# Performance work log

Measured on AMD Instinct MI355X. Metric: run time of the kernel, lower is better.

Reference implementation:

```python
import jax, jax.numpy as jnp
import numpy as np

EMBED_DIM = 1024
NUM_HEADS = 16
N = 32768


def setup_inputs() -> dict:
    key = jax.random.key(0)
    k1, k2, k3 = jax.random.split(key, 3)
    h = jax.random.normal(k1, (N, EMBED_DIM), dtype=jnp.float32)
    # torch nn.Linear(E, 3E): weight [3E, E], bias [3E] (bias=True by default)
    W_qkv = jax.random.normal(k2, (3 * EMBED_DIM, EMBED_DIM), dtype=jnp.float32) * 0.02
    b_qkv = jax.random.normal(k3, (3 * EMBED_DIM,), dtype=jnp.float32) * 0.02
    return {"h": h, "W_qkv": W_qkv, "b_qkv": b_qkv}


def reference(h, W_qkv, b_qkv):
    n, e = h.shape
    head_dim = e // NUM_HEADS
    # fused QKV projection: [N, 3E]
    qkv = h @ W_qkv.T + b_qkv
    # reshape [N, 3, H, D] -> split
    qkv = qkv.reshape(n, 3, NUM_HEADS, head_dim)
    q, k, v = qkv[:, 0], qkv[:, 1], qkv[:, 2]  # each [N, H, D]
    # NOTE: attention over the HEAD axis per token, scaled by sqrt(embed_dim)
    scores = jnp.einsum("nid,njd->nij", q, k) / (e ** 0.5)  # [N, H, H]
    attn = jax.nn.softmax(scores, axis=-1)
    out = jnp.einsum("nij,njd->nid", attn, v)  # [N, H, D]
    # faithful to torch: permute(1,0,2) then reshape(N, E) (mixes node order)
    out = jnp.transpose(out, (1, 0, 2)).reshape(n, e)
    return out
```

## Files before the change

kernel.cpp:

```cpp
#include <hip/hip_runtime.h>
#include <stdint.h>

#define NTOK 32768
#define EMB  1024
#define QKVN 3072
#define NH   16
#define HD   64

typedef __bf16 bf16x8 __attribute__((ext_vector_type(8)));
typedef float  floatx4 __attribute__((ext_vector_type(4)));
typedef unsigned int   uintx4   __attribute__((ext_vector_type(4)));
typedef unsigned short ushortx4 __attribute__((ext_vector_type(4)));
typedef unsigned short ushortx8 __attribute__((ext_vector_type(8)));

__device__ __forceinline__ unsigned short f2bf_rne(float f){
    unsigned int x; __builtin_memcpy(&x, &f, 4);
    x += 0x7fffu + ((x >> 16) & 1u);
    return (unsigned short)(x >> 16);
}

__device__ __forceinline__ void async_copy16(void* lds, const void* gsrc){
    __builtin_amdgcn_global_load_lds(
        (const __attribute__((address_space(1))) unsigned int*)gsrc,
        (__attribute__((address_space(3))) unsigned int*)lds,
        16, 0, 0);
}

__global__ __launch_bounds__(256) void cast_f32_bf16(const float* __restrict__ in,
                                                     unsigned short* __restrict__ out,
                                                     int n4){
    int idx = blockIdx.x * 256 + threadIdx.x;
    if (idx < n4){
        floatx4 v = ((const floatx4*)in)[idx];
        ushortx4 o;
        o[0] = f2bf_rne(v[0]); o[1] = f2bf_rne(v[1]);
        o[2] = f2bf_rne(v[2]); o[3] = f2bf_rne(v[3]);
        ((ushortx4*)out)[idx] = o;
    }
}

__global__ __launch_bounds__(256) void qkv_gemm(const unsigned short* __restrict__ A,
                                                const unsigned short* __restrict__ B,
                                                const float* __restrict__ bias,
                                                unsigned short* __restrict__ C){
    __shared__ unsigned short As[128 * 32];
    __shared__ unsigned short Bs[128 * 32];

    const int tid  = threadIdx.x;
    const int m0   = blockIdx.y * 128;
    const int n0   = blockIdx.x * 128;
    const int lane = tid & 63;
    const int wave = tid >> 6;
    const int wm   = (wave >> 1) * 64;
    const int wn   = (wave & 1) * 64;
    const int r16  = lane & 15;
    const int quad = lane >> 4;

    floatx4 acc[4][4];
    #pragma unroll
    for (int mi = 0; mi < 4; mi++)
        #pragma unroll
        for (int ni = 0; ni < 4; ni++)
            acc[mi][ni] = floatx4{0.f, 0.f, 0.f, 0.f};

    for (int kt = 0; kt < EMB; kt += 32){
        #pragma unroll
        for (int s = 0; s < 2; s++){
            int c   = tid + s * 256;
            int row = c >> 2;
            int k8  = (c & 3) * 8;
            async_copy16(&As[c * 8], &A[(size_t)(m0 + row) * EMB + kt + k8]);
            async_copy16(&Bs[c * 8], &B[(size_t)(n0 + row) * EMB + kt + k8]);
        }
        __syncthreads();

        bf16x8 af[4], bb[4];
        #pragma unroll
        for (int mi = 0; mi < 4; mi++)
            af[mi] = *(const bf16x8*)&As[(wm + mi * 16 + r16) * 32 + quad * 8];
        #pragma unroll
        for (int ni = 0; ni < 4; ni++)
            bb[ni] = *(const bf16x8*)&Bs[(wn + ni * 16 + r16) * 32 + quad * 8];
        #pragma unroll
        for (int mi = 0; mi < 4; mi++)
            #pragma unroll
            for (int ni = 0; ni < 4; ni++)
                acc[mi][ni] = __builtin_amdgcn_mfma_f32_16x16x32_bf16(
                                  af[mi], bb[ni], acc[mi][ni], 0, 0, 0);
        __syncthreads();
    }

    #pragma unroll
    for (int ni = 0; ni < 4; ni++){
        int gcol = n0 + wn + ni * 16 + r16;
        float bv = bias[gcol];
        #pragma unroll
        for (int mi = 0; mi < 4; mi++){
            #pragma unroll
            for (int r = 0; r < 4; r++){
                int grow = m0 + wm + mi * 16 + quad * 4 + r;
                C[(size_t)grow * QKVN + gcol] = f2bf_rne(acc[mi][ni][r] + bv);
            }
        }
    }
}

#define TOKL 3072
#define KOFF 0
#define VOFF 1152
#define POFF 2688

__global__ __launch_bounds__(256) void attn_mfma(const unsigned short* __restrict__ qkv,
                                                 float* __restrict__ out){
    __shared__ unsigned short sm[4 * TOKL];

    const int tid = threadIdx.x;
    const int n0  = blockIdx.x * 4;

    #pragma unroll
    for (int s = 0; s < 2; s++){
        int c   = tid + s * 256;
        int t   = c >> 7;
        int rem = c & 127;
        int j   = rem >> 3;
        int d8  = (rem & 7) * 8;
        ushortx8 kk = *(const ushortx8*)&qkv[(size_t)(n0 + t) * QKVN + EMB + j * HD + d8];
        *(ushortx8*)&sm[t * TOKL + KOFF + j * 72 + d8] = kk;
        ushortx8 vv = *(const ushortx8*)&qkv[(size_t)(n0 + t) * QKVN + 2 * EMB + j * HD + d8];
        #pragma unroll
        for (int e = 0; e < 8; e++)
            sm[t * TOKL + VOFF + (d8 + e) * 24 + j] = vv[e];
    }
    __syncthreads();

    const int wave = tid >> 6;
    const int lane = tid & 63;
    const int col  = lane & 15;
    const int quad = lane >> 4;
    const int n    = n0 + wave;
    unsigned short* tb = &sm[wave * TOKL];

    const unsigned short* qrow = qkv + (size_t)n * QKVN + col * HD;
    bf16x8 qf0 = *(const bf16x8*)(qrow + quad * 8);
    bf16x8 qf1 = *(const bf16x8*)(qrow + 32 + quad * 8);
    bf16x8 kf0 = *(const bf16x8*)&tb[KOFF + col * 72 + quad * 8];
    bf16x8 kf1 = *(const bf16x8*)&tb[KOFF + col * 72 + 32 + quad * 8];

    floatx4 sAcc = floatx4{0.f, 0.f, 0.f, 0.f};
    sAcc = __builtin_amdgcn_mfma_f32_16x16x32_bf16(qf0, kf0, sAcc, 0, 0, 0);
    sAcc = __builtin_amdgcn_mfma_f32_16x16x32_bf16(qf1, kf1, sAcc, 0, 0, 0);

    #pragma unroll
    for (int r = 0; r < 4; r++){
        float sv = sAcc[r] * 0.03125f;
        float m = sv;
        m = fmaxf(m, __shfl_xor(m, 1));
        m = fmaxf(m, __shfl_xor(m, 2));
        m = fmaxf(m, __shfl_xor(m, 4));
        m = fmaxf(m, __shfl_xor(m, 8));
        float p = __expf(sv - m);
        float l = p;
        l += __shfl_xor(l, 1);
        l += __shfl_xor(l, 2);
        l += __shfl_xor(l, 4);
        l += __shfl_xor(l, 8);
        p *= 1.f / l;
        tb[POFF + (quad * 4 + r) * 24 + col] = f2bf_rne(p);
    }

    bf16x8 pf;
    #pragma unroll
    for (int z = 0; z < 8; z++) pf[z] = (__bf16)0.0f;
    if (quad < 2) pf = *(const bf16x8*)&tb[POFF + col * 24 + quad * 8];

    #pragma unroll
    for (int dblk = 0; dblk < 4; dblk++){
        bf16x8 vf;
        #pragma unroll
        for (int z = 0; z < 8; z++) vf[z] = (__bf16)0.0f;
        if (quad < 2) vf = *(const bf16x8*)&tb[VOFF + (dblk * 16 + col) * 24 + quad * 8];
        floatx4 o = __builtin_amdgcn_mfma_f32_16x16x32_bf16(
                        pf, vf, floatx4{0.f, 0.f, 0.f, 0.f}, 0, 0, 0);
        #pragma unroll
        for (int r = 0; r < 4; r++){
            int i = quad * 4 + r;
            out[(size_t)i * (NTOK * HD) + (size_t)n * HD + dblk * 16 + col] = o[r];
        }
    }
}

extern "C" void kernel_launch(void* const* d_in, const int* in_sizes, int n_in,
                              void* d_out, int out_size, void* d_ws, size_t ws_size,
                              hipStream_t stream){
    const float* h = (const float*)d_in[0];
    const float* W = (const float*)d_in[1];
    const float* b = (const float*)d_in[2];
    float* out = (float*)d_out;

    char* ws = (char*)d_ws;
    unsigned short* h_bf = (unsigned short*)ws;
    unsigned short* w_bf = (unsigned short*)(ws + (size_t)64 * 1024 * 1024);
    unsigned short* qkv  = (unsigned short*)(ws + (size_t)72 * 1024 * 1024);

    cast_f32_bf16<<<(NTOK * EMB / 4 + 255) / 256, 256, 0, stream>>>(h, h_bf, NTOK * EMB / 4);
    cast_f32_bf16<<<(QKVN * EMB / 4 + 255) / 256, 256, 0, stream>>>(W, w_bf, QKVN * EMB / 4);

    dim3 ggrid(QKVN / 128, NTOK / 128);
    qkv_gemm<<<ggrid, 256, 0, stream>>>(h_bf, w_bf, b, qkv);

    attn_mfma<<<NTOK / 4, 256, 0, stream>>>(qkv, out);
}
```

Before: 524.3 us.

## Replace QKV GEMM with 256x256 double-buffered pipelined MFMA kernel

Swaps the 128x128 single-buffered GEMM for a 256x256-tile kernel with 512 threads, BK=64, XOR-swizzled LDS, and double-buffered async global-to-LDS loads. Loads are interleaved with MFMA phases under s_setprio, and the block order is swizzled for L2 locality. The aim is to hide global memory latency and cut LDS bank conflicts in the main GEMM. In exchange it uses 128KB of dynamic LDS and hand-written waitcnt and barrier scheduling that is fragile to get right.

```diff
diff --git a/kernel.cpp b/kernel.cpp
--- a/kernel.cpp
+++ b/kernel.cpp
@@ -39,66 +39,167 @@
     }
 }
 
-__global__ __launch_bounds__(256) void qkv_gemm(const unsigned short* __restrict__ A,
-                                                const unsigned short* __restrict__ B,
-                                                const float* __restrict__ bias,
-                                                unsigned short* __restrict__ C){
-    __shared__ unsigned short As[128 * 32];
-    __shared__ unsigned short Bs[128 * 32];
-
-    const int tid  = threadIdx.x;
-    const int m0   = blockIdx.y * 128;
-    const int n0   = blockIdx.x * 128;
+
+__device__ __forceinline__ void stage_a_half(unsigned short* At, const unsigned short* A,
+                                             int m0, int h, int kt, int tid){
+    #pragma unroll
+    for (int g = 0; g < 2; g++){
+        int row0  = g * 128 + h * 64;
+        int rl    = tid >> 3;
+        int chunk = tid & 7;
+        int row   = row0 + rl;
+        int k8    = chunk ^ (row & 7);
+        async_copy16((char*)At + row0 * 128 + tid * 16,
+                     &A[(size_t)(m0 + row) * EMB + kt + k8 * 8]);
+    }
+}
+
+__device__ __forceinline__ void stage_b_half(unsigned short* Bt, const unsigned short* B,
+                                             int n0, int h, int kt, int tid){
+    #pragma unroll
+    for (int j = 0; j < 2; j++){
+        int qg    = j * 2 + (tid >> 8);
+        int row0  = qg * 64 + h * 32;
+        int t2    = tid & 255;
+        int rl    = t2 >> 3;
+        int chunk = tid & 7;
+        int row   = row0 + rl;
+        int k8    = chunk ^ (row & 7);
+        async_copy16((char*)Bt + row0 * 128 + t2 * 16,
+                     &B[(size_t)(n0 + row) * EMB + kt + k8 * 8]);
+    }
+}
+
+#define LDA_HALF(H)                                                                 \
+    _Pragma("unroll")                                                               \
+    for (int mi = 0; mi < 4; mi++){                                                 \
+        int row = wm * 128 + (H) * 64 + mi * 16 + r16;                              \
+        _Pragma("unroll")                                                           \
+        for (int ks = 0; ks < 2; ks++)                                              \
+            a[mi][ks] = *(const bf16x8*)&curA[row * 64 + (((quad + 4*ks) ^ (row & 7)) * 8)]; \
+    }
+
+#define LDB_PAIR(NI0)                                                               \
+    _Pragma("unroll")                                                               \
+    for (int ni = 0; ni < 2; ni++){                                                 \
+        int row = wn * 64 + ((NI0) + ni) * 16 + r16;                                \
+        _Pragma("unroll")                                                           \
+        for (int ks = 0; ks < 2; ks++)                                              \
+            b[ni][ks] = *(const bf16x8*)&curB[row * 64 + (((quad + 4*ks) ^ (row & 7)) * 8)]; \
+    }
+
+#define MFMA16(MI0, NI0)                                                            \
+    _Pragma("unroll")                                                               \
+    for (int mi = 0; mi < 4; mi++)                                                  \
+        _Pragma("unroll")                                                           \
+        for (int ni = 0; ni < 2; ni++)                                              \
+            _Pragma("unroll")                                                       \
+            for (int ks = 0; ks < 2; ks++)                                          \
+                acc[(MI0) + mi][(NI0) + ni] = __builtin_amdgcn_mfma_f32_16x16x32_bf16( \
+                    a[mi][ks], b[ni][ks], acc[(MI0) + mi][(NI0) + ni], 0, 0, 0);
+
+__device__ __forceinline__ void ktile_iter(const unsigned short* __restrict__ A,
+                                           const unsigned short* __restrict__ B,
+                                           unsigned short* curA, unsigned short* curB,
+                                           unsigned short* nxtA, unsigned short* nxtB,
+                                           int m0, int n0, int kt, int tid,
+                                           floatx4 (&acc)[8][4]){
     const int lane = tid & 63;
     const int wave = tid >> 6;
-    const int wm   = (wave >> 1) * 64;
-    const int wn   = (wave & 1) * 64;
-    const int r16  = lane & 15;
-    const int quad = lane >> 4;
-
-    floatx4 acc[4][4];
-    #pragma unroll
-    for (int mi = 0; mi < 4; mi++)
-        #pragma unroll
-        for (int ni = 0; ni < 4; ni++)
-            acc[mi][ni] = floatx4{0.f, 0.f, 0.f, 0.f};
-
-    for (int kt = 0; kt < EMB; kt += 32){
-        #pragma unroll
-        for (int s = 0; s < 2; s++){
-            int c   = tid + s * 256;
-            int row = c >> 2;
-            int k8  = (c & 3) * 8;
-            async_copy16(&As[c * 8], &A[(size_t)(m0 + row) * EMB + kt + k8]);
-            async_copy16(&Bs[c * 8], &B[(size_t)(n0 + row) * EMB + kt + k8]);
-        }
-        __syncthreads();
-
-        bf16x8 af[4], bb[4];
-        #pragma unroll
-        for (int mi = 0; mi < 4; mi++)
-            af[mi] = *(const bf16x8*)&As[(wm + mi * 16 + r16) * 32 + quad * 8];
-        #pragma unroll
-        for (int ni = 0; ni < 4; ni++)
-            bb[ni] = *(const bf16x8*)&Bs[(wn + ni * 16 + r16) * 32 + quad * 8];
-        #pragma unroll
-        for (int mi = 0; mi < 4; mi++)
-            #pragma unroll
-            for (int ni = 0; ni < 4; ni++)
-                acc[mi][ni] = __builtin_amdgcn_mfma_f32_16x16x32_bf16(
-                                  af[mi], bb[ni], acc[mi][ni], 0, 0, 0);
-        __syncthreads();
-    }
-
+    const int wm = wave >> 2, wn = wave & 3;
+    const int r16 = lane & 15, quad = lane >> 4;
+    bf16x8 a[4][2], b[2][2];
+
+    LDA_HALF(0);
+    LDB_PAIR(0);
+    stage_a_half(nxtA, A, m0, 1, kt + 64, tid);
+    __builtin_amdgcn_s_barrier();
+    asm volatile("s_waitcnt lgkmcnt(0)" ::: "memory");
+    __builtin_amdgcn_s_setprio(1);
+    MFMA16(0, 0);
+    __builtin_amdgcn_s_setprio(0);
+    __builtin_amdgcn_s_barrier();
+
+    LDB_PAIR(2);
+    stage_b_half(nxtB, B, n0, 0, kt + 64, tid);
+    __builtin_amdgcn_s_barrier();
+    asm volatile("s_waitcnt lgkmcnt(0)" ::: "memory");
+    __builtin_amdgcn_s_setprio(1);
+    MFMA16(0, 2);
+    __builtin_amdgcn_s_setprio(0);
+    __builtin_amdgcn_s_barrier();
+
+    LDA_HALF(1);
+    stage_a_half(curA, A, m0, 0, kt + 128, tid);
+    __builtin_amdgcn_s_barrier();
+    asm volatile("s_waitcnt lgkmcnt(0)" ::: "memory");
+    __builtin_amdgcn_s_setprio(1);
+    MFMA16(4, 2);
+    __builtin_amdgcn_s_setprio(0);
+    __builtin_amdgcn_s_barrier();
+
+    LDB_PAIR(0);
+    stage_b_half(curB, B, n0, 1, kt + 128, tid);
+    __builtin_amdgcn_s_barrier();
+    asm volatile("s_waitcnt lgkmcnt(0)" ::: "memory");
+    __builtin_amdgcn_s_setprio(1);
+    MFMA16(4, 0);
+    __builtin_amdgcn_s_setprio(0);
+    asm volatile("s_waitcnt vmcnt(4)" ::: "memory");
+    __builtin_amdgcn_s_barrier();
+}
+
+__global__ __launch_bounds__(512, 2) void qkv_gemm256(const unsigned short* __restrict__ A,
+                                                      const unsigned short* __restrict__ B,
+                                                      const float* __restrict__ bias,
+                                                      unsigned short* __restrict__ C){
+    extern __shared__ __align__(16) unsigned short lds[];
+    unsigned short* A0 = lds;
+    unsigned short* B0 = lds + 16384;
+    unsigned short* A1 = lds + 32768;
+    unsigned short* B1 = lds + 49152;
+
+    const int tid = threadIdx.x;
+    int bid = blockIdx.x;
+    int swz = (bid & 7) * 192 + (bid >> 3);
+    int by  = swz / 12;
+    int bx  = swz - by * 12;
+    const int m0 = by * 256, n0 = bx * 256;
+
+    floatx4 acc[8][4];
+    #pragma unroll
+    for (int i = 0; i < 8; i++)
+        #pragma unroll
+        for (int j = 0; j < 4; j++) acc[i][j] = floatx4{0.f, 0.f, 0.f, 0.f};
+
+    stage_a_half(A0, A, m0, 0, 0, tid);
+    stage_a_half(A0, A, m0, 1, 0, tid);
+    stage_b_half(B0, B, n0, 0, 0, tid);
+    stage_b_half(B0, B, n0, 1, 0, tid);
+    stage_a_half(A1, A, m0, 0, 64, tid);
+    stage_b_half(B1, B, n0, 1, 64, tid);
+    asm volatile("s_waitcnt vmcnt(4)" ::: "memory");
+    __builtin_amdgcn_s_barrier();
+
+    #pragma unroll 1
+    for (int t = 0; t < 16; t += 2){
+        ktile_iter(A, B, A0, B0, A1, B1, m0, n0, t * 64,      tid, acc);
+        ktile_iter(A, B, A1, B1, A0, B0, m0, n0, t * 64 + 64, tid, acc);
+    }
+
+    const int lane = tid & 63;
+    const int wave = tid >> 6;
+    const int wm = wave >> 2, wn = wave & 3;
+    const int r16 = lane & 15, quad = lane >> 4;
     #pragma unroll
     for (int ni = 0; ni < 4; ni++){
-        int gcol = n0 + wn + ni * 16 + r16;
+        int gcol = n0 + wn * 64 + ni * 16 + r16;
         float bv = bias[gcol];
         #pragma unroll
-        for (int mi = 0; mi < 4; mi++){
+        for (int mi = 0; mi < 8; mi++){
             #pragma unroll
             for (int r = 0; r < 4; r++){
-                int grow = m0 + wm + mi * 16 + quad * 4 + r;
+                int grow = m0 + wm * 128 + mi * 16 + quad * 4 + r;
                 C[(size_t)grow * QKVN + gcol] = f2bf_rne(acc[mi][ni][r] + bv);
             }
         }
@@ -202,11 +303,17 @@
     unsigned short* w_bf = (unsigned short*)(ws + (size_t)64 * 1024 * 1024);
     unsigned short* qkv  = (unsigned short*)(ws + (size_t)72 * 1024 * 1024);
 
+    static bool attr_set = false;
+    if (!attr_set){
+        hipFuncSetAttribute(reinterpret_cast<const void*>(qkv_gemm256),
+                            hipFuncAttributeMaxDynamicSharedMemorySize, 131072);
+        attr_set = true;
+    }
+
     cast_f32_bf16<<<(NTOK * EMB / 4 + 255) / 256, 256, 0, stream>>>(h, h_bf, NTOK * EMB / 4);
     cast_f32_bf16<<<(QKVN * EMB / 4 + 255) / 256, 256, 0, stream>>>(W, w_bf, QKVN * EMB / 4);
 
-    dim3 ggrid(QKVN / 128, NTOK / 128);
-    qkv_gemm<<<ggrid, 256, 0, stream>>>(h_bf, w_bf, b, qkv);
+    qkv_gemm256<<<dim3(1536), 512, 131072, stream>>>(h_bf, w_bf, b, qkv);
 
     attn_mfma<<<NTOK / 4, 256, 0, stream>>>(qkv, out);
 }
```

Result: no change. 521.9 us (-0.5%).
